# Optimization experiments

Measured on AMD Instinct MI355X. Metric: run time of the kernel, lower is better.

Reference implementation:

```python
import jax, jax.numpy as jnp
import numpy as np

E = 1024      # embed_size
H = 16        # heads
D = E // H    # head_dim = 64
FF = 4 * E    # forward_expansion * embed_size
B = 2
S = 2048
LN_EPS = 1e-5


def setup_inputs() -> dict:
    key = jax.random.key(0)
    ks = jax.random.split(key, 16)
    sc = 0.02
    inp = {
        'value': jax.random.normal(ks[0], (B, S, E), jnp.float32),
        'key':   jax.random.normal(ks[1], (B, S, E), jnp.float32),
        'query': jax.random.normal(ks[2], (B, S, E), jnp.float32),
        # causal mask, broadcast over batch and heads; 0 => masked
        'mask': jnp.tril(jnp.ones((S, S), jnp.int32))[None, None],
        # fc_out: Linear(E, E)
        'Wo': jax.random.normal(ks[3], (E, E), jnp.float32) * sc,
        'bo': jnp.zeros((E,), jnp.float32),
        # pH gate: Linear(E, E)
        'Wg': jax.random.normal(ks[4], (E, E), jnp.float32) * sc,
        'bg': jnp.zeros((E,), jnp.float32),
        # LayerNorms
        'g1': jnp.ones((E,), jnp.float32), 'b1': jnp.zeros((E,), jnp.float32),
        'g2': jnp.ones((E,), jnp.float32), 'b2': jnp.zeros((E,), jnp.float32),
        # FFN
        'W1': jax.random.normal(ks[5], (E, FF), jnp.float32) * sc,
        'bf1': jnp.zeros((FF,), jnp.float32),
        'W2': jax.random.normal(ks[6], (FF, E), jnp.float32) * sc,
        'bf2': jnp.zeros((E,), jnp.float32),
    }
    return inp


def layer_norm(x, g, b):
    mu = jnp.mean(x, axis=-1, keepdims=True)
    var = jnp.mean(jnp.square(x - mu), axis=-1, keepdims=True)
    return (x - mu) * jax.lax.rsqrt(var + LN_EPS) * g + b


def reference(value, key, query, mask, Wo, bo, Wg, bg, g1, b1, g2, b2, W1, bf1, W2, bf2):
    N, seq_len, _ = query.shape
    # NOTE: original module defines per-head Linear(values/keys/queries) but never
    # applies them in forward; faithful reference omits them too.
    v = value.reshape(N, seq_len, H, D).transpose(0, 2, 1, 3)  # nhkd
    k = key.reshape(N, seq_len, H, D).transpose(0, 2, 1, 3)
    q = query.reshape(N, seq_len, H, D).transpose(0, 2, 1, 3)  # nhqd

    energy = jnp.einsum('nhqd,nhkd->nhqk', q, k)
    energy = jnp.where(mask == 0, jnp.float32(-1e20), energy)
    # faithful: mask applied BEFORE scaling by 1/sqrt(head_dim)
    attention = jax.nn.softmax(energy / jnp.sqrt(jnp.float32(D)), axis=-1)
    out = jnp.einsum('nhqk,nhkd->nhqd', attention, v)
    out = out.transpose(0, 2, 1, 3).reshape(N, seq_len, E)
    attn_output = out @ Wo + bo

    x_avg = jnp.mean(query, axis=1, keepdims=True)       # (N,1,E)
    gate = jax.nn.sigmoid(x_avg @ Wg + bg)               # (N,1,E)
    gated = gate * attn_output

    x = layer_norm(gated + query, g1, b1)                # dropout p=0 -> identity
    ff = jax.nn.gelu(x @ W1 + bf1, approximate=False) @ W2 + bf2
    out_final = layer_norm(ff + x, g2, b2)
    return out_final
```

## Files before the change

kernel.cpp:

```cpp
#include <hip/hip_runtime.h>
#include <hip/hip_bf16.h>

#define S_LEN 2048
#define EMB   1024
#define NH    16
#define HD    64
#define FF_DIM 4096
#define BATCH 2

typedef __attribute__((ext_vector_type(8))) short bf16x8;
typedef __attribute__((ext_vector_type(4))) float f32x4;

__device__ __forceinline__ short f2bf(float x) {
  __hip_bfloat16 h = (__hip_bfloat16)x;
  return *(short*)&h;
}
__device__ __forceinline__ bf16x8 pack8(float4 a, float4 b) {
  bf16x8 o;
  o[0] = f2bf(a.x); o[1] = f2bf(a.y); o[2] = f2bf(a.z); o[3] = f2bf(a.w);
  o[4] = f2bf(b.x); o[5] = f2bf(b.y); o[6] = f2bf(b.z); o[7] = f2bf(b.w);
  return o;
}

__device__ __forceinline__ void gl2lds16(const void* g, void* l) {
  __builtin_amdgcn_global_load_lds(
      (const __attribute__((address_space(1))) unsigned*)g,
      (__attribute__((address_space(3))) unsigned*)l, 16, 0, 0);
}

__device__ __forceinline__ void transpose_tile(
    const float* in, short* outS, int R, int C, int bx, int by, int t) {
  __shared__ short Ts[64][65];
  int cb = bx * 64, rb = by * 64;
  for (int idx = t; idx < 4096; idx += 256) {
    int r = idx >> 6, c = idx & 63;
    Ts[r][c] = f2bf(in[(size_t)(rb + r) * C + cb + c]);
  }
  __syncthreads();
  for (int idx = t; idx < 4096; idx += 256) {
    int oc = idx >> 6, orr = idx & 63;
    outS[(size_t)(cb + oc) * R + rb + orr] = Ts[orr][oc];
  }
}

__global__ __launch_bounds__(256) void transpose_all(
    const float* __restrict__ Wo, const float* __restrict__ W1,
    const float* __restrict__ W2, __hip_bfloat16* __restrict__ WoT,
    __hip_bfloat16* __restrict__ W1T, __hip_bfloat16* __restrict__ W2T) {
  int id = blockIdx.x, t = threadIdx.x;
  if (id < 256)        transpose_tile(Wo, (short*)WoT, EMB, EMB,    id & 15,          id >> 4,          t);
  else if (id < 1280)  transpose_tile(W1, (short*)W1T, EMB, FF_DIM, (id - 256) & 63,  (id - 256) >> 6,  t);
  else                 transpose_tile(W2, (short*)W2T, FF_DIM, EMB, (id - 1280) & 15, (id - 1280) >> 4, t);
}

__global__ __launch_bounds__(256) void zero_f32(float* __restrict__ p) {
  p[blockIdx.x * 256 + threadIdx.x] = 0.f;
}

__global__ __launch_bounds__(256) void xavg_partial(
    const float* __restrict__ Q, float* __restrict__ xavg) {
  int b = blockIdx.y;
  int s0 = blockIdx.x * 16;
  int t = threadIdx.x;
  const float* base = Q + ((size_t)b * S_LEN + s0) * EMB + 4 * t;
  float4 acc = {0.f, 0.f, 0.f, 0.f};
#pragma unroll 4
  for (int r = 0; r < 16; r++) {
    float4 v = *(const float4*)(base + (size_t)r * EMB);
    acc.x += v.x; acc.y += v.y; acc.z += v.z; acc.w += v.w;
  }
  float* dst = xavg + b * EMB + 4 * t;
  const float inv = 1.f / (float)S_LEN;
  atomicAdd(dst + 0, acc.x * inv);
  atomicAdd(dst + 1, acc.y * inv);
  atomicAdd(dst + 2, acc.z * inv);
  atomicAdd(dst + 3, acc.w * inv);
}

__global__ __launch_bounds__(256) void gate_kernel(
    const float* __restrict__ xavg, const float* __restrict__ Wg,
    const float* __restrict__ bg, float* __restrict__ gate) {
  __shared__ float red[4][64];
  int b = blockIdx.y;
  int nl = threadIdx.x & 63;
  int n = blockIdx.x * 64 + nl;
  int kg = threadIdx.x >> 6;
  const float* xa = xavg + b * EMB;
  float s = 0.f;
#pragma unroll 4
  for (int k = kg * 256; k < kg * 256 + 256; k++)
    s += xa[k] * Wg[(size_t)k * EMB + n];
  red[kg][nl] = s;
  __syncthreads();
  if (kg == 0) {
    float tot = red[0][nl] + red[1][nl] + red[2][nl] + red[3][nl] + bg[n];
    gate[b * EMB + n] = 1.f / (1.f + __expf(-tot));
  }
}

__global__ __launch_bounds__(256) void pack_kv(
    const float* __restrict__ Kg, const float* __restrict__ Vg,
    __hip_bfloat16* __restrict__ Kp, __hip_bfloat16* __restrict__ Vt) {
  __shared__ short Vs[64][72];
  int s0 = blockIdx.x * 64, h = blockIdx.y, b = blockIdx.z;
  int t = threadIdx.x, r = t >> 2, c = (t & 3) * 16;
  size_t gin = ((size_t)b * S_LEN + s0 + r) * EMB + h * HD + c;
  {
    float4 a0 = *(const float4*)(Kg + gin);
    float4 a1 = *(const float4*)(Kg + gin + 4);
    float4 a2 = *(const float4*)(Kg + gin + 8);
    float4 a3 = *(const float4*)(Kg + gin + 12);
    short* kp = (short*)Kp + (((size_t)b * NH + h) * S_LEN + s0 + r) * HD + c;
    *(bf16x8*)(kp)     = pack8(a0, a1);
    *(bf16x8*)(kp + 8) = pack8(a2, a3);
  }
  {
    float4 a0 = *(const float4*)(Vg + gin);
    float4 a1 = *(const float4*)(Vg + gin + 4);
    float4 a2 = *(const float4*)(Vg + gin + 8);
    float4 a3 = *(const float4*)(Vg + gin + 12);
    *(bf16x8*)&Vs[r][c]     = pack8(a0, a1);
    *(bf16x8*)&Vs[r][c + 8] = pack8(a2, a3);
  }
  __syncthreads();
  bf16x8 o0, o1;
#pragma unroll
  for (int j = 0; j < 8; j++) o0[j] = Vs[c + j][r];
#pragma unroll
  for (int j = 0; j < 8; j++) o1[j] = Vs[c + 8 + j][r];
  short* vp = (short*)Vt + (((size_t)b * NH + h) * HD + r) * S_LEN + s0 + c;
  *(bf16x8*)(vp)     = o0;
  *(bf16x8*)(vp + 8) = o1;
}

__global__ __launch_bounds__(256) void flash_attn_mfma(
    const float* __restrict__ Q, const __hip_bfloat16* __restrict__ Kp,
    const __hip_bfloat16* __restrict__ Vtb, __hip_bfloat16* __restrict__ O) {
  __shared__ short Ks[64][72];
  __shared__ short Vt[64][72];
  __shared__ short Ps[4][16][72];
  int t = threadIdx.x;
  int w = t >> 6, lane = t & 63, quad = lane >> 4, l15 = lane & 15;
  int j = blockIdx.x;
  int p = j & 255, g = j >> 8;
  int bh = p & 31, c_ = p >> 5;
  int qb = (g == 0) ? c_ : (g == 1) ? (15 - c_) : (g == 2) ? (16 + c_) : (31 - c_);
  int h = bh & 15, b = bh >> 4;
  size_t base = ((size_t)b * S_LEN) * EMB + h * HD;
  const short* kpb = (const short*)Kp + ((size_t)b * NH + h) * S_LEN * HD;
  const short* vtb = (const short*)Vtb + ((size_t)b * NH + h) * HD * S_LEN;

  bf16x8 qf[2];
  {
    const float* qrow = Q + base + (size_t)(qb * 64 + w * 16 + l15) * EMB;
#pragma unroll
    for (int kc = 0; kc < 2; kc++) {
      float4 a = *(const float4*)(qrow + kc * 32 + quad * 8);
      float4 c = *(const float4*)(qrow + kc * 32 + quad * 8 + 4);
      a.x *= 0.125f; a.y *= 0.125f; a.z *= 0.125f; a.w *= 0.125f;
      c.x *= 0.125f; c.y *= 0.125f; c.z *= 0.125f; c.w *= 0.125f;
      qf[kc] = pack8(a, c);
    }
  }

  f32x4 acc[4];
  float lsum[4];
  f32x4 zero = {0.f, 0.f, 0.f, 0.f};
#pragma unroll
  for (int n = 0; n < 4; n++) acc[n] = zero;
#pragma unroll
  for (int r = 0; r < 4; r++) lsum[r] = 0.f;

  int r0 = t >> 2, c0 = (t & 3) * 16;
  bf16x8 kf0, kf1, vf0, vf1;
  {
    const short* kr = kpb + (size_t)r0 * HD + c0;
    kf0 = *(const bf16x8*)(kr); kf1 = *(const bf16x8*)(kr + 8);
    const short* vr = vtb + (size_t)r0 * S_LEN + c0;
    vf0 = *(const bf16x8*)(vr); vf1 = *(const bf16x8*)(vr + 8);
  }

  for (int kt = 0; kt <= qb; kt++) {
    __syncthreads();
    *(bf16x8*)&Ks[r0][c0]     = kf0;
    *(bf16x8*)&Ks[r0][c0 + 8] = kf1;
    *(bf16x8*)&Vt[r0][c0]     = vf0;
    *(bf16x8*)&Vt[r0][c0 + 8] = vf1;
    __syncthreads();
    if (kt < qb) {
      const short* kr = kpb + (size_t)((kt + 1) * 64 + r0) * HD + c0;
      kf0 = *(const bf16x8*)(kr); kf1 = *(const bf16x8*)(kr + 8);
      const short* vr = vtb + (size_t)r0 * S_LEN + (kt + 1) * 64 + c0;
      vf0 = *(const bf16x8*)(vr); vf1 = *(const bf16x8*)(vr + 8);
    }

    f32x4 sc[4];
#pragma unroll
    for (int n = 0; n < 4; n++) sc[n] = zero;
#pragma unroll
    for (int n = 0; n < 4; n++)
#pragma unroll
      for (int kc = 0; kc < 2; kc++) {
        bf16x8 kf = *(const bf16x8*)&Ks[n * 16 + l15][kc * 32 + quad * 8];
        sc[n] = __builtin_amdgcn_mfma_f32_16x16x32_bf16(qf[kc], kf, sc[n], 0, 0, 0);
      }

    bool diag = (kt == qb);
#pragma unroll
    for (int r = 0; r < 4; r++) {
      float p0 = __expf(sc[0][r]);
      float p1 = __expf(sc[1][r]);
      float p2 = __expf(sc[2][r]);
      float p3 = __expf(sc[3][r]);
      if (diag) {
        int rowL = w * 16 + quad * 4 + r;
        if (l15      > rowL) p0 = 0.f;
        if (l15 + 16 > rowL) p1 = 0.f;
        if (l15 + 32 > rowL) p2 = 0.f;
        if (l15 + 48 > rowL) p3 = 0.f;
      }
      lsum[r] += (p0 + p1) + (p2 + p3);
      short* prow = &Ps[w][quad * 4 + r][l15];
      prow[0]  = f2bf(p0);
      prow[16] = f2bf(p1);
      prow[32] = f2bf(p2);
      prow[48] = f2bf(p3);
    }
    asm volatile("s_waitcnt lgkmcnt(0)" ::: "memory");

    bf16x8 pf0 = *(const bf16x8*)&Ps[w][l15][quad * 8];
    bf16x8 pf1 = *(const bf16x8*)&Ps[w][l15][32 + quad * 8];
#pragma unroll
    for (int n = 0; n < 4; n++) {
      bf16x8 vfa = *(const bf16x8*)&Vt[n * 16 + l15][quad * 8];
      acc[n] = __builtin_amdgcn_mfma_f32_16x16x32_bf16(pf0, vfa, acc[n], 0, 0, 0);
      bf16x8 vfb = *(const bf16x8*)&Vt[n * 16 + l15][32 + quad * 8];
      acc[n] = __builtin_amdgcn_mfma_f32_16x16x32_bf16(pf1, vfb, acc[n], 0, 0, 0);
    }
  }

#pragma unroll
  for (int r = 0; r < 4; r++) {
    float l = lsum[r];
#pragma unroll
    for (int off = 1; off < 16; off <<= 1) l += __shfl_xor(l, off);
    float invl = 1.f / l;
    size_t orow = base + (size_t)(qb * 64 + w * 16 + quad * 4 + r) * EMB;
#pragma unroll
    for (int n = 0; n < 4; n++)
      O[orow + n * 16 + l15] = (__hip_bfloat16)(acc[n][r] * invl);
  }
}

template <int MODE, int TM>
__global__ __launch_bounds__(256) void gemm_bt(
    const __hip_bfloat16* __restrict__ A, const __hip_bfloat16* __restrict__ BT,
    int K, int N, const float* __restrict__ bias,
    const float* __restrict__ gate, const float* __restrict__ residF,
    const __hip_bfloat16* __restrict__ residB,
    float* __restrict__ outF, __hip_bfloat16* __restrict__ outB) {
  constexpr int MI = TM / 32;
  constexpr int AR = TM / 32;
  __shared__ short As[2][TM][64];
  __shared__ short Bs[2][128][64];
  int t = threadIdx.x;
  int w = t >> 6, lane = t & 63, quad = lane >> 4, l15 = lane & 15;
  int wm = (w >> 1) * (TM / 2), wn = (w & 1) * 64;
  int mBase = blockIdx.y * TM, nBase = blockIdx.x * 128;
  f32x4 acc[MI][4];
  f32x4 zero = {0.f, 0.f, 0.f, 0.f};
#pragma unroll
  for (int i = 0; i < MI; i++)
#pragma unroll
    for (int j = 0; j < 4; j++) acc[i][j] = zero;
  const short* Ag = (const short*)A;
  const short* Bg = (const short*)BT;

  int rl = t >> 3;
  int sck = t & 7;
  int wrow = w << 3;

  auto stage = [&](int buf, int kt) {
    int kb = kt << 6;
#pragma unroll
    for (int rd = 0; rd < AR; rd++) {
      int R = (rd << 5) + rl;
      gl2lds16(&Ag[(size_t)(mBase + R) * K + kb + ((sck ^ (R & 7)) << 3)],
               &As[buf][(rd << 5) + wrow][0]);
    }
#pragma unroll
    for (int rd = 0; rd < 4; rd++) {
      int R = (rd << 5) + rl;
      gl2lds16(&Bg[(size_t)(nBase + R) * K + kb + ((sck ^ (R & 7)) << 3)],
               &Bs[buf][(rd << 5) + wrow][0]);
    }
  };

  const int nt = K >> 6;
  stage(0, 0);
  __syncthreads();
  int cur = 0;
  for (int kt = 0; kt < nt; kt++) {
    if (kt + 1 < nt) stage(cur ^ 1, kt + 1);
#pragma unroll
    for (int kh = 0; kh < 2; kh++) {
      bf16x8 af[MI], bfr[4];
      int dch = (kh << 2) + quad;
#pragma unroll
      for (int mi = 0; mi < MI; mi++) {
        int R = wm + mi * 16 + l15;
        af[mi] = *(const bf16x8*)&As[cur][R][(dch ^ (R & 7)) << 3];
      }
#pragma unroll
      for (int ni = 0; ni < 4; ni++) {
        int R = wn + ni * 16 + l15;
        bfr[ni] = *(const bf16x8*)&Bs[cur][R][(dch ^ (R & 7)) << 3];
      }
      __builtin_amdgcn_s_setprio(1);
#pragma unroll
      for (int mi = 0; mi < MI; mi++)
#pragma unroll
        for (int ni = 0; ni < 4; ni++)
          acc[mi][ni] = __builtin_amdgcn_mfma_f32_16x16x32_bf16(af[mi], bfr[ni], acc[mi][ni], 0, 0, 0);
      __builtin_amdgcn_s_setprio(0);
    }
    __syncthreads();
    cur ^= 1;
  }

#pragma unroll
  for (int mi = 0; mi < MI; mi++) {
#pragma unroll
    for (int r = 0; r < 4; r++) {
      int row = mBase + wm + mi * 16 + quad * 4 + r;
#pragma unroll
      for (int ni = 0; ni < 4; ni++) {
        int col = nBase + wn + ni * 16 + l15;
        float v = acc[mi][ni][r];
        if (MODE == 0) {
          float g = gate[(row >> 11) * EMB + col];
          v = g * (v + bias[col]) + residF[(size_t)row * N + col];
          outF[(size_t)row * N + col] = v;
        } else if (MODE == 1) {
          v += bias[col];
          v = 0.5f * v * (1.0f + erff(v * 0.70710678118654752f));
          outB[(size_t)row * N + col] = (__hip_bfloat16)v;
        } else {
          v += bias[col] + (float)residB[(size_t)row * N + col];
          outF[(size_t)row * N + col] = v;
        }
      }
    }
  }
}

__device__ __forceinline__ float block_sum_256(float v) {
  __shared__ float sb[4];
#pragma unroll
  for (int off = 32; off > 0; off >>= 1) v += __shfl_down(v, off);
  int w = threadIdx.x >> 6, ln = threadIdx.x & 63;
  if (ln == 0) sb[w] = v;
  __syncthreads();
  float r = sb[0] + sb[1] + sb[2] + sb[3];
  __syncthreads();
  return r;
}

template <bool TO_BF16>
__global__ __launch_bounds__(256) void ln_kernel(
    const float* __restrict__ y, const float* __restrict__ g,
    const float* __restrict__ b, __hip_bfloat16* __restrict__ outB,
    float* __restrict__ outF) {
  size_t row = blockIdx.x;
  const float* yr = y + row * EMB;
  float v[4];
#pragma unroll
  for (int i = 0; i < 4; i++) v[i] = yr[threadIdx.x + i * 256];
  float s = block_sum_256(v[0] + v[1] + v[2] + v[3]);
  float mu = s * (1.f / (float)EMB);
  float q = 0.f;
#pragma unroll
  for (int i = 0; i < 4; i++) { float d = v[i] - mu; q += d * d; }
  q = block_sum_256(q);
  float rs = rsqrtf(q * (1.f / (float)EMB) + 1e-5f);
#pragma unroll
  for (int i = 0; i < 4; i++) {
    int e = threadIdx.x + i * 256;
    float o = (v[i] - mu) * rs * g[e] + b[e];
    if (TO_BF16) outB[row * EMB + e] = (__hip_bfloat16)o;
    else         outF[row * EMB + e] = o;
  }
}

extern "C" void kernel_launch(void* const* d_in, const int* in_sizes, int n_in,
                              void* d_out, int out_size, void* d_ws, size_t ws_size,
                              hipStream_t stream) {
  const float* Val = (const float*)d_in[0];
  const float* Key = (const float*)d_in[1];
  const float* Qry = (const float*)d_in[2];
  const float* Wo  = (const float*)d_in[4];
  const float* bo  = (const float*)d_in[5];
  const float* Wg  = (const float*)d_in[6];
  const float* bg  = (const float*)d_in[7];
  const float* g1  = (const float*)d_in[8];
  const float* b1  = (const float*)d_in[9];
  const float* g2  = (const float*)d_in[10];
  const float* b2  = (const float*)d_in[11];
  const float* W1  = (const float*)d_in[12];
  const float* bf1 = (const float*)d_in[13];
  const float* W2  = (const float*)d_in[14];
  const float* bf2 = (const float*)d_in[15];
  float* out = (float*)d_out;

  char* ws = (char*)d_ws;
  size_t off = 0;
  auto alloc = [&](size_t bytes) {
    char* p = ws + off;
    off += (bytes + 255) & ~(size_t)255;
    return p;
  };
  const size_t MB = 1024 * 1024;
  bool bigws = ws_size >= 78 * MB;

  __hip_bfloat16* WoT = (__hip_bfloat16*)alloc((size_t)EMB * EMB * 2);
  __hip_bfloat16* W1T = (__hip_bfloat16*)alloc((size_t)EMB * FF_DIM * 2);
  __hip_bfloat16* W2T = (__hip_bfloat16*)alloc((size_t)EMB * FF_DIM * 2);
  size_t kvRegion = bigws ? (size_t)BATCH * S_LEN * FF_DIM * 2
                          : (size_t)S_LEN * FF_DIM * 2;
  char* kvBase = alloc(kvRegion);
  __hip_bfloat16* Kpk  = (__hip_bfloat16*)kvBase;
  __hip_bfloat16* Vtb  = (__hip_bfloat16*)(kvBase + 8 * MB);
  __hip_bfloat16* Hbuf = (__hip_bfloat16*)kvBase;
  __hip_bfloat16* attnO = (__hip_bfloat16*)alloc((size_t)BATCH * S_LEN * EMB * 2);
  float* ybuf = (float*)alloc((size_t)BATCH * S_LEN * EMB * 4);
  float* xavg = (float*)alloc(BATCH * EMB * 4);
  float* gate = (float*)alloc(BATCH * EMB * 4);
  __hip_bfloat16* xb = attnO;
  float* zbuf = ybuf;

  transpose_all<<<2304, 256, 0, stream>>>(Wo, W1, W2, WoT, W1T, W2T);
  zero_f32<<<BATCH * EMB / 256, 256, 0, stream>>>(xavg);
  xavg_partial<<<dim3(128, BATCH), 256, 0, stream>>>(Qry, xavg);
  gate_kernel<<<dim3(16, BATCH), 256, 0, stream>>>(xavg, Wg, bg, gate);
  pack_kv<<<dim3(32, NH, BATCH), 256, 0, stream>>>(Key, Val, Kpk, Vtb);
  flash_attn_mfma<<<1024, 256, 0, stream>>>(Qry, Kpk, Vtb, attnO);
  gemm_bt<0, 64><<<dim3(8, 64), 256, 0, stream>>>(attnO, WoT, EMB, EMB, bo, gate, Qry, nullptr, ybuf, nullptr);
  ln_kernel<true><<<4096, 256, 0, stream>>>(ybuf, g1, b1, xb, nullptr);
  if (bigws) {
    gemm_bt<1, 128><<<dim3(32, 32), 256, 0, stream>>>(xb, W1T, EMB, FF_DIM, bf1, nullptr, nullptr, nullptr, nullptr, Hbuf);
    gemm_bt<2, 64><<<dim3(8, 64), 256, 0, stream>>>(Hbuf, W2T, FF_DIM, EMB, bf2, nullptr, nullptr, xb, zbuf, nullptr);
  } else {
    for (int b = 0; b < BATCH; b++) {
      const __hip_bfloat16* xbb = xb + (size_t)b * S_LEN * EMB;
      gemm_bt<1, 128><<<dim3(32, 16), 256, 0, stream>>>(xbb, W1T, EMB, FF_DIM, bf1, nullptr, nullptr, nullptr, nullptr, Hbuf);
      gemm_bt<2, 64><<<dim3(8, 32), 256, 0, stream>>>(Hbuf, W2T, FF_DIM, EMB, bf2, nullptr, nullptr, xbb,
                                                      zbuf + (size_t)b * S_LEN * EMB, nullptr);
    }
  }
  ln_kernel<false><<<4096, 256, 0, stream>>>(zbuf, g2, b2, nullptr, out);
}
```

Before: 414.3 us.

## Add 256x256 eight-wave pipelined GEMM for FFN1 and enlarge FFN2 tile

Adds a new 512-thread GEMM kernel for the first FFN layer. It uses 256x256 output tiles, XOR-swizzled LDS, direct global-to-LDS loads, a double buffer with prefetch interleaved between four MFMA phases, setprio around the MFMAs, and a block-index swizzle. GELU and bias are fused into its epilogue. The aim is more data reuse per tile and better overlap of memory and MFMA work than the old 128-row tile. The FFN2 GEMM moves from TM=64 to TM=128, which halves its block count in exchange for more per-block reuse. The hand-written waitcnt and barrier schedule is fragile, and with only 256 blocks the launch may not fill all CUs well.

```diff
diff --git a/kernel.cpp b/kernel.cpp
--- a/kernel.cpp
+++ b/kernel.cpp
@@ -27,6 +27,14 @@
       (const __attribute__((address_space(1))) unsigned*)g,
       (__attribute__((address_space(3))) unsigned*)l, 16, 0, 0);
 }
+
+__device__ __forceinline__ void bar() {
+  asm volatile("" ::: "memory");
+  __builtin_amdgcn_s_barrier();
+  asm volatile("" ::: "memory");
+}
+#define WAITVM(n) asm volatile("s_waitcnt vmcnt(" #n ")" ::: "memory")
+#define LGKM0     asm volatile("s_waitcnt lgkmcnt(0)" ::: "memory")
 
 __device__ __forceinline__ void transpose_tile(
     const float* in, short* outS, int R, int C, int bx, int by, int t) {
@@ -249,6 +257,137 @@
 #pragma unroll
     for (int n = 0; n < 4; n++)
       O[orow + n * 16 + l15] = (__hip_bfloat16)(acc[n][r] * invl);
+  }
+}
+
+#define MFMA_QUAD(MH, NHq)                                                       \
+  __builtin_amdgcn_s_setprio(1);                                                 \
+  _Pragma("unroll") for (int mi_ = 0; mi_ < 4; mi_++)                            \
+  _Pragma("unroll") for (int ni_ = 0; ni_ < 2; ni_++)                            \
+  _Pragma("unroll") for (int kh_ = 0; kh_ < 2; kh_++)                            \
+    acc[(MH) * 4 + mi_][(NHq) * 2 + ni_] = __builtin_amdgcn_mfma_f32_16x16x32_bf16( \
+        af[mi_][kh_], bfr[(NHq) * 2 + ni_][kh_], acc[(MH) * 4 + mi_][(NHq) * 2 + ni_], 0, 0, 0); \
+  __builtin_amdgcn_s_setprio(0);
+
+__global__ __launch_bounds__(512) void gemm8p_gelu(
+    const __hip_bfloat16* __restrict__ A, const __hip_bfloat16* __restrict__ BT,
+    int K, int N, const float* __restrict__ bias, __hip_bfloat16* __restrict__ outB) {
+  __shared__ short As[2][256][64];
+  __shared__ short Bs[2][256][64];
+  int t = threadIdx.x;
+  int w = t >> 6, lane = t & 63, quad = lane >> 4, l15 = lane & 15;
+  int warp_m = w >> 2, warp_n = w & 3;
+  int cpx = gridDim.x >> 3;
+  int swz = ((int)blockIdx.x & 7) * cpx + ((int)blockIdx.x >> 3);
+  int nbn = N >> 8;
+  int mBase = (swz / nbn) << 8, nBase = (swz % nbn) << 8;
+  const short* Ag = (const short*)A;
+  const short* Bg = (const short*)BT;
+  int sck = t & 7;
+  int rr = t >> 3;
+  int wrow = w << 3;
+
+  auto stA = [&](int buf, int kt, int h) {
+    int kb = kt << 6;
+#pragma unroll
+    for (int rd = 0; rd < 2; rd++) {
+      int R = h * 128 + rd * 64 + rr;
+      gl2lds16(&Ag[(size_t)(mBase + R) * K + kb + ((sck ^ (R & 7)) << 3)],
+               &As[buf][h * 128 + rd * 64 + wrow][0]);
+    }
+  };
+  auto stB = [&](int buf, int kt, int h) {
+    int kb = kt << 6;
+#pragma unroll
+    for (int rd = 0; rd < 2; rd++) {
+      int R = h * 128 + rd * 64 + rr;
+      gl2lds16(&Bg[(size_t)(nBase + R) * K + kb + ((sck ^ (R & 7)) << 3)],
+               &Bs[buf][h * 128 + rd * 64 + wrow][0]);
+    }
+  };
+
+  f32x4 acc[8][4];
+  f32x4 zero = {0.f, 0.f, 0.f, 0.f};
+#pragma unroll
+  for (int i = 0; i < 8; i++)
+#pragma unroll
+    for (int j = 0; j < 4; j++) acc[i][j] = zero;
+
+  const int nt = K >> 6;
+  stA(0, 0, 0); stA(0, 0, 1); stB(0, 0, 0); stB(0, 0, 1);
+  stA(1, 1, 0); stA(1, 1, 1); stB(1, 1, 0); stB(1, 1, 1);
+  WAITVM(8);
+  bar();
+
+  bf16x8 af[4][2], bfr[4][2];
+  for (int kt = 0; kt < nt; kt++) {
+    const int buf = kt & 1;
+    const bool pre = (kt + 2 < nt);
+#pragma unroll
+    for (int mi = 0; mi < 4; mi++) {
+      int R = warp_m * 128 + mi * 16 + l15;
+#pragma unroll
+      for (int kh = 0; kh < 2; kh++)
+        af[mi][kh] = *(const bf16x8*)&As[buf][R][((kh * 4 + quad) ^ (R & 7)) << 3];
+    }
+#pragma unroll
+    for (int ni = 0; ni < 2; ni++) {
+      int R = warp_n * 64 + ni * 16 + l15;
+#pragma unroll
+      for (int kh = 0; kh < 2; kh++)
+        bfr[ni][kh] = *(const bf16x8*)&Bs[buf][R][((kh * 4 + quad) ^ (R & 7)) << 3];
+    }
+    bar();
+    LGKM0;
+    MFMA_QUAD(0, 0);
+    bar();
+#pragma unroll
+    for (int ni = 2; ni < 4; ni++) {
+      int R = warp_n * 64 + ni * 16 + l15;
+#pragma unroll
+      for (int kh = 0; kh < 2; kh++)
+        bfr[ni][kh] = *(const bf16x8*)&Bs[buf][R][((kh * 4 + quad) ^ (R & 7)) << 3];
+    }
+    bar();
+    LGKM0;
+    MFMA_QUAD(0, 1);
+    bar();
+#pragma unroll
+    for (int mi = 0; mi < 4; mi++) {
+      int R = warp_m * 128 + (4 + mi) * 16 + l15;
+#pragma unroll
+      for (int kh = 0; kh < 2; kh++)
+        af[mi][kh] = *(const bf16x8*)&As[buf][R][((kh * 4 + quad) ^ (R & 7)) << 3];
+    }
+    if (pre) { stB(buf, kt + 2, 0); stB(buf, kt + 2, 1); }
+    bar();
+    LGKM0;
+    MFMA_QUAD(1, 0);
+    bar();
+    if (pre) { stA(buf, kt + 2, 0); stA(buf, kt + 2, 1); }
+    bar();
+    LGKM0;
+    MFMA_QUAD(1, 1);
+    if (pre) { WAITVM(8); } else { WAITVM(0); }
+    bar();
+  }
+
+  float bcol[4];
+#pragma unroll
+  for (int ni = 0; ni < 4; ni++) bcol[ni] = bias[nBase + warp_n * 64 + ni * 16 + l15];
+#pragma unroll
+  for (int mi = 0; mi < 8; mi++) {
+#pragma unroll
+    for (int r = 0; r < 4; r++) {
+      int row = mBase + warp_m * 128 + mi * 16 + quad * 4 + r;
+#pragma unroll
+      for (int ni = 0; ni < 4; ni++) {
+        int col = nBase + warp_n * 64 + ni * 16 + l15;
+        float v = acc[mi][ni][r] + bcol[ni];
+        v = 0.5f * v * (1.0f + erff(v * 0.70710678118654752f));
+        outB[(size_t)row * N + col] = (__hip_bfloat16)v;
+      }
+    }
   }
 }
 
@@ -447,14 +586,14 @@
   gemm_bt<0, 64><<<dim3(8, 64), 256, 0, stream>>>(attnO, WoT, EMB, EMB, bo, gate, Qry, nullptr, ybuf, nullptr);
   ln_kernel<true><<<4096, 256, 0, stream>>>(ybuf, g1, b1, xb, nullptr);
   if (bigws) {
-    gemm_bt<1, 128><<<dim3(32, 32), 256, 0, stream>>>(xb, W1T, EMB, FF_DIM, bf1, nullptr, nullptr, nullptr, nullptr, Hbuf);
-    gemm_bt<2, 64><<<dim3(8, 64), 256, 0, stream>>>(Hbuf, W2T, FF_DIM, EMB, bf2, nullptr, nullptr, xb, zbuf, nullptr);
+    gemm8p_gelu<<<256, 512, 0, stream>>>(xb, W1T, EMB, FF_DIM, bf1, Hbuf);
+    gemm_bt<2, 128><<<dim3(8, 32), 256, 0, stream>>>(Hbuf, W2T, FF_DIM, EMB, bf2, nullptr, nullptr, xb, zbuf, nullptr);
   } else {
     for (int b = 0; b < BATCH; b++) {
       const __hip_bfloat16* xbb = xb + (size_t)b * S_LEN * EMB;
       gemm_bt<1, 128><<<dim3(32, 16), 256, 0, stream>>>(xbb, W1T, EMB, FF_DIM, bf1, nullptr, nullptr, nullptr, nullptr, Hbuf);
-      gemm_bt<2, 64><<<dim3(8, 32), 256, 0, stream>>>(Hbuf, W2T, FF_DIM, EMB, bf2, nullptr, nullptr, xbb,
-                                                      zbuf + (size_t)b * S_LEN * EMB, nullptr);
+      gemm_bt<2, 128><<<dim3(8, 16), 256, 0, stream>>>(Hbuf, W2T, FF_DIM, EMB, bf2, nullptr, nullptr, xbb,
+                                                       zbuf + (size_t)b * S_LEN * EMB, nullptr);
     }
   }
   ln_kernel<false><<<4096, 256, 0, stream>>>(zbuf, g2, b2, nullptr, out);
```

Measured after the change: 428.9 us. 1.04x slower.
